# Performance work log

Hardware: AMD Instinct MI355X
Metric: run time of the kernel (lower is better)

## Reference

```python
import jax, jax.numpy as jnp
import numpy as np
import jax.lax as lax

CHANNELS = 3
SCALE = 0.25
SIGMA = (1.0 / SCALE - 1.0) / 2.0          # 1.5
KSIZE = 2 * round(SIGMA * 4) + 1           # 13
KA = KSIZE // 2                            # 6
KB = KA if KSIZE % 2 == 1 else KA - 1      # 6
INT_INV_SCALE = int(1.0 / SCALE)           # 4


def _gaussian_kernel():
    # 2D Gaussian as outer product of identical 1D Gaussians, normalized to sum 1
    coords = np.arange(KSIZE, dtype=np.float32)
    mean = (KSIZE - 1) / 2.0
    g1 = np.exp(-((coords - mean) ** 2) / (2.0 * SIGMA ** 2))
    k2 = np.outer(g1, g1)
    k2 = k2 / k2.sum()
    # depthwise weight layout OIHW with O=channels, I=1
    w = np.broadcast_to(k2[None, None], (CHANNELS, 1, KSIZE, KSIZE)).astype(np.float32)
    return jnp.asarray(w)


def setup_inputs() -> dict:
    key = jax.random.key(0)
    inp = jax.random.normal(key, (32, CHANNELS, 512, 512), dtype=jnp.float32)
    weight = _gaussian_kernel()
    return {"inp": inp, "weight": weight}


def reference(inp, weight):
    # F.pad(ka, kb, ka, kb) + depthwise conv + out[:, :, ::s, ::s]
    # is exactly a strided depthwise conv with explicit (ka, kb) padding,
    # since the subsample starts at index 0.
    out = lax.conv_general_dilated(
        inp, weight,
        window_strides=(INT_INV_SCALE, INT_INV_SCALE),
        padding=[(KA, KB), (KA, KB)],
        feature_group_count=CHANNELS,
        dimension_numbers=("NCHW", "OIHW", "NCHW"),
    )
    return out  # [32, 3, 128, 128]
```

## Files before the change

kernel.cpp:

```cpp
#include <hip/hip_runtime.h>


constexpr int N_IMG = 32, CH = 3, H = 512, W = 512;
constexpr int OH = 128, OW = 128;
constexpr int KS = 13, KA = 6, STR = 4;
constexpr int TILE_R = 8;
constexpr int IN_ROWS = TILE_R * STR + (KS - STR);
constexpr int WCH = W / 4;

__global__ __launch_bounds__(256)
void aa_interp_kernel(const float* __restrict__ in,
                      const float* __restrict__ wgt,
                      float* __restrict__ out) {
    __shared__ float hsh[KS];
    __shared__ float hbuf[IN_ROWS][OW];

    const int nc  = blockIdx.y;
    const int r0  = blockIdx.x * TILE_R;
    const int tid = threadIdx.x;

    if (tid < KS) {
        const float* w2 = wgt + (size_t)(nc % CH) * KS * KS + (size_t)tid * KS;
        float s = 0.f;
        #pragma unroll
        for (int j = 0; j < KS; ++j) s += w2[j];
        hsh[tid] = s;
    }
    __syncthreads();

    float h[KS];
    #pragma unroll
    for (int k = 0; k < KS; ++k) h[k] = hsh[k];

    const float* inp = in + (size_t)nc * H * W;
    const int gr0 = r0 * STR - KA;

    for (int idx = tid; idx < IN_ROWS * OW; idx += 256) {
        const int ir = idx >> 7;
        const int oc = idx & (OW - 1);
        const int gr = gr0 + ir;
        float acc = 0.f;
        if (gr >= 0 && gr < H) {
            const float4* row = (const float4*)(inp + (size_t)gr * W);
            float f[16];
            #pragma unroll
            for (int q = 0; q < 4; ++q) {
                const int cq  = oc - 2 + q;
                const int cqc = min(max(cq, 0), WCH - 1);
                const float4 c = row[cqc];
                const bool ok = (cq == cqc);
                f[4 * q + 0] = ok ? c.x : 0.f;
                f[4 * q + 1] = ok ? c.y : 0.f;
                f[4 * q + 2] = ok ? c.z : 0.f;
                f[4 * q + 3] = ok ? c.w : 0.f;
            }
            #pragma unroll
            for (int k = 0; k < KS; ++k) acc += h[k] * f[k + 2];
        }
        hbuf[ir][oc] = acc;
    }
    __syncthreads();

    float* op = out + (size_t)nc * OH * OW;
    {
        const int orow = tid >> 5;
        const int oc4  = tid & 31;
        float4 acc = make_float4(0.f, 0.f, 0.f, 0.f);
        #pragma unroll
        for (int k = 0; k < KS; ++k) {
            const float4 t = *(const float4*)&hbuf[orow * STR + k][4 * oc4];
            acc.x += h[k] * t.x; acc.y += h[k] * t.y;
            acc.z += h[k] * t.z; acc.w += h[k] * t.w;
        }
        *((float4*)(op + (size_t)(r0 + orow) * OW) + oc4) = acc;
    }
}

extern "C" void kernel_launch(void* const* d_in, const int* in_sizes, int n_in,
                              void* d_out, int out_size, void* d_ws, size_t ws_size,
                              hipStream_t stream) {
    const float* in  = (const float*)d_in[0];
    const float* wgt = (const float*)d_in[1];
    float* out = (float*)d_out;

    dim3 grid(OH / TILE_R, N_IMG * CH);
    aa_interp_kernel<<<grid, dim3(256), 0, stream>>>(in, wgt, out);
}
```

Measured before the change: 155.3 us.

## Split fused separable blur into separate horizontal and vertical pass kernels

Replaces the single fused kernel, which kept horizontally filtered rows in shared memory, with two kernels. A horizontal pass writes the full per-image intermediate (all 512 rows × 128 columns) to the workspace, and a vertical pass reads it back to produce the output. This removes the recomputation of overlapping halo rows between tiles and the shared-memory barrier. In exchange it adds a round trip through global memory for a 25 MB intermediate and a second launch.

```diff
diff --git a/kernel.cpp b/kernel.cpp
--- a/kernel.cpp
+++ b/kernel.cpp
@@ -1,30 +1,27 @@
 #include <hip/hip_runtime.h>
 
 
-constexpr int N_IMG = 32, CH = 3, H = 512, W = 512;
+constexpr int CH = 3, H = 512, W = 512;
 constexpr int OH = 128, OW = 128;
 constexpr int KS = 13, KA = 6, STR = 4;
-constexpr int TILE_R = 8;
-constexpr int IN_ROWS = TILE_R * STR + (KS - STR);
+constexpr int HW1 = H * OW;
 constexpr int WCH = W / 4;
 
 __global__ __launch_bounds__(256)
-void aa_interp_kernel(const float* __restrict__ in,
-                      const float* __restrict__ wgt,
-                      float* __restrict__ out) {
+void aa_hpass(const float* __restrict__ in, const float* __restrict__ wgt,
+              float* __restrict__ hbuf) {
     __shared__ float hsh[KS];
-    __shared__ float hbuf[IN_ROWS][OW];
+    const int gid = blockIdx.x * 256 + threadIdx.x;
+    const int oc  = gid & (OW - 1);
+    const int ir  = (gid >> 7) & (H - 1);
+    const int nc  = gid >> 16;
 
-    const int nc  = blockIdx.y;
-    const int r0  = blockIdx.x * TILE_R;
-    const int tid = threadIdx.x;
-
-    if (tid < KS) {
-        const float* w2 = wgt + (size_t)(nc % CH) * KS * KS + (size_t)tid * KS;
+    if (threadIdx.x < KS) {
+        const float* w2 = wgt + (nc % CH) * KS * KS + (int)threadIdx.x * KS;
         float s = 0.f;
         #pragma unroll
         for (int j = 0; j < KS; ++j) s += w2[j];
-        hsh[tid] = s;
+        hsh[threadIdx.x] = s;
     }
     __syncthreads();
 
@@ -32,48 +29,57 @@
     #pragma unroll
     for (int k = 0; k < KS; ++k) h[k] = hsh[k];
 
-    const float* inp = in + (size_t)nc * H * W;
-    const int gr0 = r0 * STR - KA;
+    const float4* row = (const float4*)(in + ((size_t)nc * H + ir) * W);
+    float f[16];
+    #pragma unroll
+    for (int q = 0; q < 4; ++q) {
+        const int cq  = oc - 2 + q;
+        const int cqc = min(max(cq, 0), WCH - 1);
+        const float4 c = row[cqc];
+        const bool ok = (cq == cqc);
+        f[4 * q + 0] = ok ? c.x : 0.f;
+        f[4 * q + 1] = ok ? c.y : 0.f;
+        f[4 * q + 2] = ok ? c.z : 0.f;
+        f[4 * q + 3] = ok ? c.w : 0.f;
+    }
+    float a = 0.f;
+    #pragma unroll
+    for (int k = 0; k < KS; ++k) a += h[k] * f[k + 2];
+    hbuf[gid] = a;
+}
 
-    for (int idx = tid; idx < IN_ROWS * OW; idx += 256) {
-        const int ir = idx >> 7;
-        const int oc = idx & (OW - 1);
-        const int gr = gr0 + ir;
-        float acc = 0.f;
-        if (gr >= 0 && gr < H) {
-            const float4* row = (const float4*)(inp + (size_t)gr * W);
-            float f[16];
-            #pragma unroll
-            for (int q = 0; q < 4; ++q) {
-                const int cq  = oc - 2 + q;
-                const int cqc = min(max(cq, 0), WCH - 1);
-                const float4 c = row[cqc];
-                const bool ok = (cq == cqc);
-                f[4 * q + 0] = ok ? c.x : 0.f;
-                f[4 * q + 1] = ok ? c.y : 0.f;
-                f[4 * q + 2] = ok ? c.z : 0.f;
-                f[4 * q + 3] = ok ? c.w : 0.f;
-            }
-            #pragma unroll
-            for (int k = 0; k < KS; ++k) acc += h[k] * f[k + 2];
-        }
-        hbuf[ir][oc] = acc;
+__global__ __launch_bounds__(256)
+void aa_vpass(const float* __restrict__ hbuf, const float* __restrict__ wgt,
+              float* __restrict__ out) {
+    __shared__ float hsh[KS];
+    const int gid  = blockIdx.x * 256 + threadIdx.x;
+    const int oc   = gid & (OW - 1);
+    const int orow = (gid >> 7) & (OH - 1);
+    const int nc   = gid >> 14;
+
+    if (threadIdx.x < KS) {
+        const float* w2 = wgt + (nc % CH) * KS * KS + (int)threadIdx.x * KS;
+        float s = 0.f;
+        #pragma unroll
+        for (int j = 0; j < KS; ++j) s += w2[j];
+        hsh[threadIdx.x] = s;
     }
     __syncthreads();
 
-    float* op = out + (size_t)nc * OH * OW;
-    {
-        const int orow = tid >> 5;
-        const int oc4  = tid & 31;
-        float4 acc = make_float4(0.f, 0.f, 0.f, 0.f);
-        #pragma unroll
-        for (int k = 0; k < KS; ++k) {
-            const float4 t = *(const float4*)&hbuf[orow * STR + k][4 * oc4];
-            acc.x += h[k] * t.x; acc.y += h[k] * t.y;
-            acc.z += h[k] * t.z; acc.w += h[k] * t.w;
-        }
-        *((float4*)(op + (size_t)(r0 + orow) * OW) + oc4) = acc;
+    float h[KS];
+    #pragma unroll
+    for (int k = 0; k < KS; ++k) h[k] = hsh[k];
+
+    const float* hb = hbuf + (size_t)nc * HW1;
+    float a = 0.f;
+    #pragma unroll
+    for (int k = 0; k < KS; ++k) {
+        const int rr = STR * orow - KA + k;
+        const int rc = min(max(rr, 0), H - 1);
+        const float hk = (rr == rc) ? h[k] : 0.f;
+        a += hk * hb[rc * OW + oc];
     }
+    out[gid] = a;
 }
 
 extern "C" void kernel_launch(void* const* d_in, const int* in_sizes, int n_in,
@@ -81,8 +87,11 @@
                               hipStream_t stream) {
     const float* in  = (const float*)d_in[0];
     const float* wgt = (const float*)d_in[1];
-    float* out = (float*)d_out;
+    float* out  = (float*)d_out;
+    float* hbuf = (float*)d_ws;
 
-    dim3 grid(OH / TILE_R, N_IMG * CH);
-    aa_interp_kernel<<<grid, dim3(256), 0, stream>>>(in, wgt, out);
+    const int n1 = 32 * CH * H * OW;
+    const int n2 = 32 * CH * OH * OW;
+    aa_hpass<<<n1 / 256, 256, 0, stream>>>(in, wgt, hbuf);
+    aa_vpass<<<n2 / 256, 256, 0, stream>>>(hbuf, wgt, out);
 }
```

Result: slower. 160.8 us (+3.5%).
